# Kernel optimization log

Hardware: AMD Instinct MI355X
Metric: run time of the kernel (lower is better)

Reference implementation:

```python
import jax, jax.numpy as jnp
import numpy as np


def setup_inputs() -> dict:
    key = jax.random.key(0)
    k1, k2 = jax.random.split(key)
    N, K, D = 32768, 1024, 512
    x = jax.random.normal(k1, (N, D), dtype=jnp.float32)
    centers = jax.random.normal(k2, (K, D), dtype=jnp.float32)
    return {"x": x, "centers": centers}


def reference(x, centers):
    # broadcasted (x[:,None]-c[None])**2 sum without the O(N*K*D) intermediate)
    x_sq = jnp.sum(x * x, axis=-1, keepdims=True)           # [N, 1]
    c_sq = jnp.sum(centers * centers, axis=-1)              # [K]
    cross = jnp.einsum('nd,kd->nk', x, centers)             # [N, K]
    norm_squared = x_sq + c_sq[None, :] - 2.0 * cross       # [N, K]
    # exp(-d/2) / sum_k exp(-d/2) == softmax(-d/2) over clusters
    probabilities = jax.nn.softmax(-0.5 * norm_squared, axis=1)
    return probabilities
```

## Files before the change

### kernel.cpp

```cpp
#include <hip/hip_runtime.h>
#include <stdint.h>


namespace {
constexpr int N_ROWS  = 32768;
constexpr int K_CL    = 1024;
constexpr int D_DIM   = 512;
constexpr int BM      = 64;
constexpr int THREADS = 512;
constexpr int WAVES   = 8;
constexpr int NSLICE  = 16;
}

typedef _Float16 f16_t;
typedef _Float16 f16x8 __attribute__((ext_vector_type(8)));
typedef _Float16 f16x4 __attribute__((ext_vector_type(4)));
typedef float    f32x16 __attribute__((ext_vector_type(16)));
typedef float    f32x4v __attribute__((ext_vector_type(4)));

__global__ __launch_bounds__(64) void prep_kernel(const float* __restrict__ centers,
                                                  f16_t* __restrict__ bpack,
                                                  float* __restrict__ bias) {
  const int col = blockIdx.x, lane = threadIdx.x;
  const int t  = lane >> 2;
  const int ks = (lane >> 1) & 1;
  const int kh = lane & 1;
  const float* src = centers + (size_t)col * D_DIM + lane * 8;
  f16x8 hi;
  float ssq = 0.f;
  #pragma unroll
  for (int i = 0; i < 8; ++i) {
    float v = src[i];
    ssq += v * v;
    hi[i] = (f16_t)v;
  }
  const int jh = col >> 9, cb = (col & 511) >> 5, c32 = col & 31;
  const size_t off = ((size_t)ks * 16 + cb) * 512 + (c32 * 2 + kh) * 8;
  *(f16x8*)(bpack + (size_t)(2 * t + jh) * 16384 + off) = hi;
  for (int o = 32; o; o >>= 1) ssq += __shfl_down(ssq, o, 64);
  if (lane == 0) bias[col] = -0.5f * ssq;
}

__global__ __launch_bounds__(THREADS, 2) void cluster_kernel(
    const float* __restrict__ x, const f16_t* __restrict__ bpack,
    const float* __restrict__ bias, float* __restrict__ out) {
  __shared__ f16_t Abuf[2][4][64][8];
  __shared__ float red[WAVES * BM];
  __shared__ float fin[BM];

  const int tid  = threadIdx.x;
  const int wid  = tid >> 6;
  const int lane = tid & 63;
  const int l31  = lane & 31;
  const int h    = lane >> 5;
  const int brow = blockIdx.x * BM;
  const int xrow = tid >> 3, q8 = tid & 7;

  f32x16 acc[2][4];
  #pragma unroll
  for (int rb = 0; rb < 2; ++rb)
    #pragma unroll
    for (int cc = 0; cc < 4; ++cc)
      #pragma unroll
      for (int e = 0; e < 16; ++e) acc[rb][cc][e] = 0.f;

  const char* bbase = (const char*)bpack + wid * 2048 + (l31 * 2 + h) * 16;
  const float* xbase = x + (size_t)(brow + xrow) * D_DIM + q8 * 4;

#define LOADB(S, DST)                                                          \
  {                                                                            \
    const char* p_ = bbase + (size_t)((S) & 31) * 32768;                       \
    (DST)[0] = *(const f16x8*)(p_);                          \
    (DST)[1] = *(const f16x8*)(p_ + 1024);                   \
    (DST)[2] = *(const f16x8*)(p_ + 16384);                  \
    (DST)[3] = *(const f16x8*)(p_ + 17408);                  \
  }
#define CONVERT(XV, PAR)                                                       \
  {                                                                            \
    f16x4 h4_;                                                                 \
    h4_[0] = (f16_t)(XV)[0]; h4_[1] = (f16_t)(XV)[1];                          \
    h4_[2] = (f16_t)(XV)[2]; h4_[3] = (f16_t)(XV)[3];                          \
    *(f16x4*)&Abuf[(PAR)][q8 >> 1][xrow][(q8 & 1) * 4] = h4_;                  \
  }
#define COMPUTE(B, JH)                                                         \
  {                                                                            \
    _Pragma("unroll")                                                          \
    for (int ks_ = 0; ks_ < 2; ++ks_)                                          \
      _Pragma("unroll")                                                        \
      for (int c2_ = 0; c2_ < 2; ++c2_) {                                      \
        _Pragma("unroll")                                                      \
        for (int rb_ = 0; rb_ < 2; ++rb_)                                      \
          acc[rb_][(JH) * 2 + c2_] = __builtin_amdgcn_mfma_f32_32x32x16_f16(   \
              a[rb_][ks_], (B)[ks_ * 2 + c2_], acc[rb_][(JH) * 2 + c2_],       \
              0, 0, 0);                                                        \
      }                                                                        \
  }

  f16x8 bcur[4], bnxt[4];
  f16x8 a[2][2];

  {
    f32x4v xv0 = __builtin_nontemporal_load((const f32x4v*)xbase);
    CONVERT(xv0, 0)
  }
  LOADB(0, bcur)
  f32x4v xc = __builtin_nontemporal_load((const f32x4v*)(xbase + 32));
  __syncthreads();

  #pragma unroll 1
  for (int t = 0; t < NSLICE; ++t) {
    #pragma unroll
    for (int rb = 0; rb < 2; ++rb)
      #pragma unroll
      for (int ks = 0; ks < 2; ++ks)
        a[rb][ks] = *(const f16x8*)&Abuf[t & 1][ks * 2 + h][rb * 32 + l31][0];

    LOADB(2 * t + 1, bnxt)
    f32x4v xn = __builtin_nontemporal_load(
        (const f32x4v*)(xbase + ((t + 2) & 15) * 32));
    COMPUTE(bcur, 0)

    LOADB(2 * t + 2, bcur)
    COMPUTE(bnxt, 1)

    CONVERT(xc, (t + 1) & 1)
    __syncthreads();
    xc = xn;
  }

  float bcol[4];
  #pragma unroll
  for (int cc = 0; cc < 4; ++cc)
    bcol[cc] = bias[(cc >> 1) * 512 + wid * 64 + (cc & 1) * 32 + l31];

  float rr[2][16];
  #pragma unroll
  for (int rb = 0; rb < 2; ++rb)
    #pragma unroll
    for (int reg = 0; reg < 16; ++reg) {
      float m = -3.0e38f;
      #pragma unroll
      for (int cc = 0; cc < 4; ++cc) {
        float v = acc[rb][cc][reg] + bcol[cc];
        acc[rb][cc][reg] = v;
        m = fmaxf(m, v);
      }
      m = fmaxf(m, __shfl_xor(m, 1, 64));
      m = fmaxf(m, __shfl_xor(m, 2, 64));
      m = fmaxf(m, __shfl_xor(m, 4, 64));
      m = fmaxf(m, __shfl_xor(m, 8, 64));
      m = fmaxf(m, __shfl_xor(m, 16, 64));
      rr[rb][reg] = m;
    }
  if (l31 == 0) {
    #pragma unroll
    for (int rb = 0; rb < 2; ++rb)
      #pragma unroll
      for (int reg = 0; reg < 16; ++reg)
        red[wid * BM + rb * 32 + (reg & 3) + 8 * (reg >> 2) + 4 * h] = rr[rb][reg];
  }
  __syncthreads();
  if (tid < BM) {
    float m = red[tid];
    #pragma unroll
    for (int w = 1; w < WAVES; ++w) m = fmaxf(m, red[w * BM + tid]);
    fin[tid] = m;
  }
  __syncthreads();

  #pragma unroll
  for (int rb = 0; rb < 2; ++rb)
    #pragma unroll
    for (int reg = 0; reg < 16; ++reg) {
      const float m = fin[rb * 32 + (reg & 3) + 8 * (reg >> 2) + 4 * h];
      float s = 0.f;
      #pragma unroll
      for (int cc = 0; cc < 4; ++cc) {
        float e = __expf(acc[rb][cc][reg] - m);
        acc[rb][cc][reg] = e;
        s += e;
      }
      s += __shfl_xor(s, 1, 64);
      s += __shfl_xor(s, 2, 64);
      s += __shfl_xor(s, 4, 64);
      s += __shfl_xor(s, 8, 64);
      s += __shfl_xor(s, 16, 64);
      rr[rb][reg] = s;
    }
  __syncthreads();
  if (l31 == 0) {
    #pragma unroll
    for (int rb = 0; rb < 2; ++rb)
      #pragma unroll
      for (int reg = 0; reg < 16; ++reg)
        red[wid * BM + rb * 32 + (reg & 3) + 8 * (reg >> 2) + 4 * h] = rr[rb][reg];
  }
  __syncthreads();
  if (tid < BM) {
    float s = 0.f;
    #pragma unroll
    for (int w = 0; w < WAVES; ++w) s += red[w * BM + tid];
    fin[tid] = 1.0f / s;
  }
  __syncthreads();

  #pragma unroll
  for (int rb = 0; rb < 2; ++rb)
    #pragma unroll
    for (int reg = 0; reg < 16; ++reg) {
      const int row = rb * 32 + (reg & 3) + 8 * (reg >> 2) + 4 * h;
      const float rs = fin[row];
      #pragma unroll
      for (int cc = 0; cc < 4; ++cc) {
        const int col = (cc >> 1) * 512 + wid * 64 + (cc & 1) * 32 + l31;
        __builtin_nontemporal_store(acc[rb][cc][reg] * rs,
                                    &out[(size_t)(brow + row) * K_CL + col]);
      }
    }
}

extern "C" void kernel_launch(void* const* d_in, const int* in_sizes, int n_in,
                              void* d_out, int out_size, void* d_ws, size_t ws_size,
                              hipStream_t stream) {
  const float* x       = (const float*)d_in[0];
  const float* centers = (const float*)d_in[1];
  float* out = (float*)d_out;

  f16_t* bpack = (f16_t*)d_ws;
  float* bias  = (float*)((char*)d_ws + (size_t)32 * 32768);

  prep_kernel<<<K_CL, 64, 0, stream>>>(centers, bpack, bias);
  cluster_kernel<<<N_ROWS / BM, THREADS, 0, stream>>>(x, bpack, bias, out);
}
```

Before: 95.54 us.

## Stage full x tile in swizzled LDS and remove per-slice barriers

Loads and converts the block's entire 64x512 x tile to fp16 in shared memory up front, using an XOR swizzle to avoid bank conflicts. This removes the per-iteration syncthreads and double-buffered conversion from the MFMA loop. B fragments are now loaded in larger 8-vector double buffers and the loop is fully unrolled. The cost is a non-overlapped prologue for the x load, 64KB of LDS per block and higher register pressure.

```diff
diff --git a/kernel.cpp b/kernel.cpp
--- a/kernel.cpp
+++ b/kernel.cpp
@@ -44,7 +44,7 @@
 __global__ __launch_bounds__(THREADS, 2) void cluster_kernel(
     const float* __restrict__ x, const f16_t* __restrict__ bpack,
     const float* __restrict__ bias, float* __restrict__ out) {
-  __shared__ f16_t Abuf[2][4][64][8];
+  __shared__ __align__(16) char Ax[64 * 1024];
   __shared__ float red[WAVES * BM];
   __shared__ float fin[BM];
 
@@ -54,78 +54,93 @@
   const int l31  = lane & 31;
   const int h    = lane >> 5;
   const int brow = blockIdx.x * BM;
-  const int xrow = tid >> 3, q8 = tid & 7;
-
-  f32x16 acc[2][4];
-  #pragma unroll
-  for (int rb = 0; rb < 2; ++rb)
-    #pragma unroll
-    for (int cc = 0; cc < 4; ++cc)
-      #pragma unroll
-      for (int e = 0; e < 16; ++e) acc[rb][cc][e] = 0.f;
 
   const char* bbase = (const char*)bpack + wid * 2048 + (l31 * 2 + h) * 16;
-  const float* xbase = x + (size_t)(brow + xrow) * D_DIM + q8 * 4;
-
-#define LOADB(S, DST)                                                          \
+
+#define LOADB8(S, DST)                                                         \
   {                                                                            \
     const char* p_ = bbase + (size_t)((S) & 31) * 32768;                       \
-    (DST)[0] = *(const f16x8*)(p_);                          \
-    (DST)[1] = *(const f16x8*)(p_ + 1024);                   \
-    (DST)[2] = *(const f16x8*)(p_ + 16384);                  \
-    (DST)[3] = *(const f16x8*)(p_ + 17408);                  \
-  }
-#define CONVERT(XV, PAR)                                                       \
-  {                                                                            \
-    f16x4 h4_;                                                                 \
-    h4_[0] = (f16_t)(XV)[0]; h4_[1] = (f16_t)(XV)[1];                          \
-    h4_[2] = (f16_t)(XV)[2]; h4_[3] = (f16_t)(XV)[3];                          \
-    *(f16x4*)&Abuf[(PAR)][q8 >> 1][xrow][(q8 & 1) * 4] = h4_;                  \
-  }
-#define COMPUTE(B, JH)                                                         \
+    (DST)[0] = *(const f16x8*)(p_);                       \
+    (DST)[1] = *(const f16x8*)(p_ + 1024);                \
+    (DST)[2] = *(const f16x8*)(p_ + 16384);               \
+    (DST)[3] = *(const f16x8*)(p_ + 17408);               \
+    (DST)[4] = *(const f16x8*)(p_ + 32768);               \
+    (DST)[5] = *(const f16x8*)(p_ + 33792);               \
+    (DST)[6] = *(const f16x8*)(p_ + 49152);               \
+    (DST)[7] = *(const f16x8*)(p_ + 50176);               \
+  }
+#define COMPUTE16(B)                                                           \
   {                                                                            \
     _Pragma("unroll")                                                          \
-    for (int ks_ = 0; ks_ < 2; ++ks_)                                          \
+    for (int j2_ = 0; j2_ < 2; ++j2_)                                          \
       _Pragma("unroll")                                                        \
-      for (int c2_ = 0; c2_ < 2; ++c2_) {                                      \
+      for (int ks_ = 0; ks_ < 2; ++ks_)                                        \
         _Pragma("unroll")                                                      \
-        for (int rb_ = 0; rb_ < 2; ++rb_)                                      \
-          acc[rb_][(JH) * 2 + c2_] = __builtin_amdgcn_mfma_f32_32x32x16_f16(   \
-              a[rb_][ks_], (B)[ks_ * 2 + c2_], acc[rb_][(JH) * 2 + c2_],       \
-              0, 0, 0);                                                        \
-      }                                                                        \
-  }
-
-  f16x8 bcur[4], bnxt[4];
+        for (int c2_ = 0; c2_ < 2; ++c2_)                                      \
+          _Pragma("unroll")                                                    \
+          for (int rb_ = 0; rb_ < 2; ++rb_)                                    \
+            acc[rb_][j2_ * 2 + c2_] = __builtin_amdgcn_mfma_f32_32x32x16_f16(  \
+                a[rb_][ks_], (B)[j2_ * 4 + ks_ * 2 + c2_],                     \
+                acc[rb_][j2_ * 2 + c2_], 0, 0, 0);                             \
+  }
+
+  f16x8 bA[8], bB[8];
+
+  LOADB8(0, bA)
+
+  {
+    const float* xsrc = x + (size_t)brow * D_DIM;
+    #pragma unroll
+    for (int it = 0; it < 16; ++it) {
+      const int idx = it * 512 + tid;
+      const int r = idx >> 7, f = idx & 127;
+      f32x4v v = __builtin_nontemporal_load(
+          (const f32x4v*)(xsrc + (size_t)r * D_DIM + f * 4));
+      f16x4 h4;
+      h4[0] = (f16_t)v[0]; h4[1] = (f16_t)v[1];
+      h4[2] = (f16_t)v[2]; h4[3] = (f16_t)v[3];
+      *(f16x4*)(Ax + r * 1024 + ((f * 8) ^ ((r & 7) << 4))) = h4;
+    }
+  }
+  __syncthreads();
+
+  f32x16 acc[2][4];
+  #pragma unroll
+  for (int rb = 0; rb < 2; ++rb)
+    #pragma unroll
+    for (int cc = 0; cc < 4; ++cc)
+      #pragma unroll
+      for (int e = 0; e < 16; ++e) acc[rb][cc][e] = 0.f;
+
+  const char* abase0 = Ax + l31 * 1024;
+  const int swz = (l31 & 7) << 4;
+  const int h16 = h * 16;
   f16x8 a[2][2];
 
-  {
-    f32x4v xv0 = __builtin_nontemporal_load((const f32x4v*)xbase);
-    CONVERT(xv0, 0)
-  }
-  LOADB(0, bcur)
-  f32x4v xc = __builtin_nontemporal_load((const f32x4v*)(xbase + 32));
-  __syncthreads();
-
-  #pragma unroll 1
-  for (int t = 0; t < NSLICE; ++t) {
-    #pragma unroll
-    for (int rb = 0; rb < 2; ++rb)
-      #pragma unroll
-      for (int ks = 0; ks < 2; ++ks)
-        a[rb][ks] = *(const f16x8*)&Abuf[t & 1][ks * 2 + h][rb * 32 + l31][0];
-
-    LOADB(2 * t + 1, bnxt)
-    f32x4v xn = __builtin_nontemporal_load(
-        (const f32x4v*)(xbase + ((t + 2) & 15) * 32));
-    COMPUTE(bcur, 0)
-
-    LOADB(2 * t + 2, bcur)
-    COMPUTE(bnxt, 1)
-
-    CONVERT(xc, (t + 1) & 1)
-    __syncthreads();
-    xc = xn;
+  #pragma unroll
+  for (int tt = 0; tt < 8; ++tt) {
+    {
+      const int T = 2 * tt;
+      LOADB8(2 * (T + 1), bB)
+      const int o0 = (T * 64 + h16) ^ swz;
+      const int o1 = o0 ^ 32;
+      a[0][0] = *(const f16x8*)(abase0 + o0);
+      a[0][1] = *(const f16x8*)(abase0 + o1);
+      a[1][0] = *(const f16x8*)(abase0 + 32768 + o0);
+      a[1][1] = *(const f16x8*)(abase0 + 32768 + o1);
+      COMPUTE16(bA)
+    }
+    {
+      const int T = 2 * tt + 1;
+      if (T < 15) LOADB8(2 * (T + 1), bA)
+      const int o0 = (T * 64 + h16) ^ swz;
+      const int o1 = o0 ^ 32;
+      a[0][0] = *(const f16x8*)(abase0 + o0);
+      a[0][1] = *(const f16x8*)(abase0 + o1);
+      a[1][0] = *(const f16x8*)(abase0 + 32768 + o0);
+      a[1][1] = *(const f16x8*)(abase0 + 32768 + o1);
+      COMPUTE16(bB)
+    }
   }
 
   float bcol[4];
@@ -152,6 +167,7 @@
       m = fmaxf(m, __shfl_xor(m, 16, 64));
       rr[rb][reg] = m;
     }
+  __syncthreads();
   if (l31 == 0) {
     #pragma unroll
     for (int rb = 0; rb < 2; ++rb)
```

Result: faster. 89.23 us (-6.6%).
